# Optimization experiments

Measured on AMD Instinct MI355X. Metric: run time of the kernel, lower is better.

The kernel has to match this reference:

```python
import jax, jax.numpy as jnp
import numpy as np

NUM_FEATURES = 40960
EMB_DIM = 2048


def setup_inputs() -> dict:
    key = jax.random.key(0)
    ks = jax.random.split(key, 8)
    B, L = 4096, 32
    white = jax.random.randint(ks[0], (B, L), 0, NUM_FEATURES, dtype=jnp.int64)
    black = jax.random.randint(ks[1], (B, L), 0, NUM_FEATURES, dtype=jnp.int64)
    stm = jax.random.randint(ks[2], (B,), 0, 2, dtype=jnp.int64)
    emb_table = jax.random.normal(ks[3], (NUM_FEATURES, EMB_DIM), dtype=jnp.float32) * 0.02
    W1 = jax.random.normal(ks[4], (128, 2 * EMB_DIM), dtype=jnp.float32) * 0.02
    b1 = jax.random.normal(ks[5], (128,), dtype=jnp.float32) * 0.02
    W2 = jax.random.normal(ks[6], (1, 128), dtype=jnp.float32) * 0.02
    b2 = jax.random.normal(ks[7], (1,), dtype=jnp.float32) * 0.02
    return {"white": white, "black": black, "stm": stm,
            "emb_table": emb_table, "W1": W1, "b1": b1, "W2": W2, "b2": b2}


def _encode(emb_table, idx):
    # idx: [B, L] padded with 0; embedding gather then mask out padding (index 0)
    emb = emb_table[idx]                         # [B, L, D]
    mask = (idx != 0)[..., None].astype(emb.dtype)
    return (emb * mask).sum(axis=1)              # [B, D]


def reference(white, black, stm, emb_table, W1, b1, W2, b2):
    w = _encode(emb_table, white)                # [B, D]
    b = _encode(emb_table, black)                # [B, D]
    wb = jnp.concatenate([w, b], axis=1)         # [B, 2D]
    bw = jnp.concatenate([b, w], axis=1)
    x = jnp.where((stm == 1)[:, None], wb, bw)
    h = jax.nn.relu(x @ W1.T + b1)               # [B, 128]
    return h @ W2.T + b2                         # [B, 1]
```

## Files before the change

kernel.cpp:

```cpp
#include <hip/hip_runtime.h>
#include <cstddef>

typedef __bf16 bf16x8 __attribute__((ext_vector_type(8)));
typedef float  floatx4 __attribute__((ext_vector_type(4)));

static __device__ __forceinline__ unsigned short f2bf(float f) {
    unsigned int u = __float_as_uint(f);
    u = u + 0x7fff + ((u >> 16) & 1);
    return (unsigned short)(u >> 16);
}
static __device__ __forceinline__ float bflo(unsigned int u) {
    return __uint_as_float(u << 16);
}
static __device__ __forceinline__ float bfhi(unsigned int u) {
    return __uint_as_float(u & 0xffff0000u);
}

__global__ __launch_bounds__(256) void nnue_convw1(
    const float* __restrict__ W1, unsigned short* __restrict__ W1b)
{
    const int i = (blockIdx.x * 256 + threadIdx.x) * 4;
    const float4 v = *reinterpret_cast<const float4*>(W1 + i);
    ushort4 o;
    o.x = f2bf(v.x); o.y = f2bf(v.y); o.z = f2bf(v.z); o.w = f2bf(v.w);
    *reinterpret_cast<ushort4*>(W1b + i) = o;
}

#define LDST 72
__global__ __launch_bounds__(512) void nnue_pgemm(
    const float* __restrict__ emb, const unsigned short* __restrict__ w1b,
    unsigned short* __restrict__ P)
{
    __shared__ unsigned short As[64 * LDST];
    __shared__ unsigned short Bs[256 * LDST];

    const int t    = threadIdx.x;
    const int wid  = t >> 6;
    const int lane = t & 63;
    const int quad = lane >> 4;
    const int l16  = lane & 15;
    const int wm   = wid >> 2;
    const int wn   = wid & 3;
    const int fbase = blockIdx.x * 64;

    floatx4 acc[2][4];
#pragma unroll
    for (int i = 0; i < 2; ++i)
#pragma unroll
        for (int j = 0; j < 4; ++j) acc[i][j] = (floatx4){0.f, 0.f, 0.f, 0.f};

    for (int kc = 0; kc < 2048; kc += 64) {
        __syncthreads();
#pragma unroll
        for (int i = 0; i < 2; ++i) {
            const int c = t + i * 512;
            const int row = c >> 4, cc = c & 15;
            const float4 v = *reinterpret_cast<const float4*>(
                emb + (size_t)(fbase + row) * 2048 + kc + cc * 4);
            ushort4 o;
            o.x = f2bf(v.x); o.y = f2bf(v.y); o.z = f2bf(v.z); o.w = f2bf(v.w);
            *reinterpret_cast<ushort4*>(As + row * LDST + cc * 4) = o;
        }
#pragma unroll
        for (int i = 0; i < 4; ++i) {
            const int c = t + i * 512;
            const int row = c >> 3, cc = c & 7;
            const uint4 v = *reinterpret_cast<const uint4*>(
                w1b + (size_t)(row & 127) * 4096 + (row >> 7) * 2048 + kc + cc * 8);
            *reinterpret_cast<uint4*>(Bs + row * LDST + cc * 8) = v;
        }
        __syncthreads();
#pragma unroll
        for (int kk = 0; kk < 64; kk += 32) {
            const bf16x8 a0 = *reinterpret_cast<const bf16x8*>(
                As + (wm * 32 + l16) * LDST + kk + quad * 8);
            const bf16x8 a1 = *reinterpret_cast<const bf16x8*>(
                As + (wm * 32 + 16 + l16) * LDST + kk + quad * 8);
#pragma unroll
            for (int ni = 0; ni < 4; ++ni) {
                const bf16x8 bb = *reinterpret_cast<const bf16x8*>(
                    Bs + (wn * 64 + ni * 16 + l16) * LDST + kk + quad * 8);
                acc[0][ni] = __builtin_amdgcn_mfma_f32_16x16x32_bf16(a0, bb, acc[0][ni], 0, 0, 0);
                acc[1][ni] = __builtin_amdgcn_mfma_f32_16x16x32_bf16(a1, bb, acc[1][ni], 0, 0, 0);
            }
        }
    }

#pragma unroll
    for (int mi = 0; mi < 2; ++mi) {
#pragma unroll
        for (int ni = 0; ni < 4; ++ni) {
            const int n = wn * 64 + ni * 16 + l16;
#pragma unroll
            for (int r = 0; r < 4; ++r) {
                const int f = fbase + wm * 32 + mi * 16 + quad * 4 + r;
                P[(size_t)f * 256 + n] = f2bf(acc[mi][ni][r]);
            }
        }
    }
}

__global__ __launch_bounds__(256) void nnue_out(
    const int* __restrict__ white, const int* __restrict__ black,
    const int* __restrict__ stm, const unsigned short* __restrict__ P,
    const float* __restrict__ b1, const float* __restrict__ W2,
    const float* __restrict__ b2, float* __restrict__ out)
{
    __shared__ int sW[128], sB[128];
    const int t = threadIdx.x;
    const int bbase = blockIdx.x * 4;
    if (t < 128) sW[t] = white[bbase * 32 + t];
    else         sB[t - 128] = black[bbase * 32 + (t - 128)];
    __syncthreads();

    const int w = t >> 6, lane = t & 63;
    const int b = bbase + w;
    const int offw = (stm[b] != 0) ? 0 : 128;
    const int offb = 128 - offw;
    const int n2 = lane * 2;

    float h0 = 0.f, h1 = 0.f;
#pragma unroll
    for (int i = 0; i < 32; ++i) {
        const int iw = sW[w * 32 + i];
        const unsigned int uw = *reinterpret_cast<const unsigned int*>(
            P + (size_t)iw * 256 + offw + n2);
        const float mw = (iw != 0) ? 1.f : 0.f;
        h0 += bflo(uw) * mw;
        h1 += bfhi(uw) * mw;

        const int ib = sB[w * 32 + i];
        const unsigned int ub = *reinterpret_cast<const unsigned int*>(
            P + (size_t)ib * 256 + offb + n2);
        const float mb = (ib != 0) ? 1.f : 0.f;
        h0 += bflo(ub) * mb;
        h1 += bfhi(ub) * mb;
    }

    h0 += b1[n2];     h1 += b1[n2 + 1];
    h0 = (h0 > 0.f) ? h0 : 0.f;
    h1 = (h1 > 0.f) ? h1 : 0.f;
    float s = h0 * W2[n2] + h1 * W2[n2 + 1];
#pragma unroll
    for (int m = 1; m < 64; m <<= 1) s += __shfl_xor(s, m, 64);
    if (lane == 0) out[b] = s + b2[0];
}

extern "C" void kernel_launch(void* const* d_in, const int* in_sizes, int n_in,
                              void* d_out, int out_size, void* d_ws, size_t ws_size,
                              hipStream_t stream)
{
    const int*   white = (const int*)d_in[0];
    const int*   black = (const int*)d_in[1];
    const int*   stm   = (const int*)d_in[2];
    const float* emb   = (const float*)d_in[3];
    const float* W1    = (const float*)d_in[4];
    const float* b1    = (const float*)d_in[5];
    const float* W2    = (const float*)d_in[6];
    const float* b2    = (const float*)d_in[7];
    float* out = (float*)d_out;

    unsigned short* w1buf = (unsigned short*)d_ws;
    unsigned short* pbuf  = w1buf + (size_t)128 * 4096;

    nnue_convw1<<<512, 256, 0, stream>>>(W1, w1buf);
    nnue_pgemm<<<640, 512, 0, stream>>>(emb, w1buf, pbuf);
    nnue_out<<<1024, 256, 0, stream>>>(white, black, stm, pbuf, b1, W2, b2, out);
}
```

Measured before the change: 525.7 us.

## Retile projection GEMM to 128x128 blocks with direct-to-LDS swizzled W1 loads

```diff
diff --git a/kernel.cpp b/kernel.cpp
--- a/kernel.cpp
+++ b/kernel.cpp
@@ -26,78 +26,91 @@
     *reinterpret_cast<ushort4*>(W1b + i) = o;
 }
 
-#define LDST 72
-__global__ __launch_bounds__(512) void nnue_pgemm(
+#define ALDS 72
+__global__ __launch_bounds__(256) void nnue_pgemm(
     const float* __restrict__ emb, const unsigned short* __restrict__ w1b,
     unsigned short* __restrict__ P)
 {
-    __shared__ unsigned short As[64 * LDST];
-    __shared__ unsigned short Bs[256 * LDST];
+    __shared__ unsigned short As[128 * ALDS];
+    __shared__ unsigned short Bs[128 * 64];
 
     const int t    = threadIdx.x;
     const int wid  = t >> 6;
     const int lane = t & 63;
     const int quad = lane >> 4;
     const int l16  = lane & 15;
-    const int wm   = wid >> 2;
-    const int wn   = wid & 3;
-    const int fbase = blockIdx.x * 64;
+    const int wm   = wid >> 1;
+    const int wn   = wid & 1;
+    const int fbase = (blockIdx.x >> 1) * 128;
+    const int nblk  = blockIdx.x & 1;
 
-    floatx4 acc[2][4];
+    const int bsrc_shorts = (((lane & 7) ^ (lane >> 3)) << 3);
+    const int brow        = lane >> 3;
+
+    floatx4 acc[4][4];
 #pragma unroll
-    for (int i = 0; i < 2; ++i)
+    for (int i = 0; i < 4; ++i)
 #pragma unroll
         for (int j = 0; j < 4; ++j) acc[i][j] = (floatx4){0.f, 0.f, 0.f, 0.f};
 
     for (int kc = 0; kc < 2048; kc += 64) {
         __syncthreads();
 #pragma unroll
-        for (int i = 0; i < 2; ++i) {
-            const int c = t + i * 512;
-            const int row = c >> 4, cc = c & 15;
+        for (int i = 0; i < 4; ++i) {
+            const int c = wid * 4 + i;
+            const int r = c * 8 + brow;
+            const unsigned short* g = w1b + (size_t)r * 4096 + nblk * 2048
+                                    + kc + bsrc_shorts;
+            auto* dst = (__attribute__((address_space(3))) unsigned int*)(Bs + c * 512);
+            __builtin_amdgcn_global_load_lds(
+                (const __attribute__((address_space(1))) unsigned int*)g,
+                dst, 16, 0, 0);
+        }
+#pragma unroll
+        for (int i = 0; i < 8; ++i) {
+            const int cch = t + i * 256;
+            const int row = cch >> 4, cc = cch & 15;
             const float4 v = *reinterpret_cast<const float4*>(
                 emb + (size_t)(fbase + row) * 2048 + kc + cc * 4);
             ushort4 o;
             o.x = f2bf(v.x); o.y = f2bf(v.y); o.z = f2bf(v.z); o.w = f2bf(v.w);
-            *reinterpret_cast<ushort4*>(As + row * LDST + cc * 4) = o;
-        }
-#pragma unroll
-        for (int i = 0; i < 4; ++i) {
-            const int c = t + i * 512;
-            const int row = c >> 3, cc = c & 7;
-            const uint4 v = *reinterpret_cast<const uint4*>(
-                w1b + (size_t)(row & 127) * 4096 + (row >> 7) * 2048 + kc + cc * 8);
-            *reinterpret_cast<uint4*>(Bs + row * LDST + cc * 8) = v;
+            *reinterpret_cast<ushort4*>(As + row * ALDS + cc * 4) = o;
         }
         __syncthreads();
 #pragma unroll
         for (int kk = 0; kk < 64; kk += 32) {
-            const bf16x8 a0 = *reinterpret_cast<const bf16x8*>(
-                As + (wm * 32 + l16) * LDST + kk + quad * 8);
-            const bf16x8 a1 = *reinterpret_cast<const bf16x8*>(
-                As + (wm * 32 + 16 + l16) * LDST + kk + quad * 8);
+            bf16x8 a[4], b[4];
+#pragma unroll
+            for (int mi = 0; mi < 4; ++mi)
+                a[mi] = *reinterpret_cast<const bf16x8*>(
+                    As + (wm * 64 + mi * 16 + l16) * ALDS + kk + quad * 8);
 #pragma unroll
             for (int ni = 0; ni < 4; ++ni) {
-                const bf16x8 bb = *reinterpret_cast<const bf16x8*>(
-                    Bs + (wn * 64 + ni * 16 + l16) * LDST + kk + quad * 8);
-                acc[0][ni] = __builtin_amdgcn_mfma_f32_16x16x32_bf16(a0, bb, acc[0][ni], 0, 0, 0);
-                acc[1][ni] = __builtin_amdgcn_mfma_f32_16x16x32_bf16(a1, bb, acc[1][ni], 0, 0, 0);
+                const int r  = wn * 64 + ni * 16 + l16;
+                const int cb = (kk * 2 + quad * 16) ^ ((r & 7) << 4);
+                b[ni] = *reinterpret_cast<const bf16x8*>(
+                    reinterpret_cast<const char*>(Bs) + r * 128 + cb);
             }
+#pragma unroll
+            for (int mi = 0; mi < 4; ++mi)
+#pragma unroll
+                for (int ni = 0; ni < 4; ++ni)
+                    acc[mi][ni] = __builtin_amdgcn_mfma_f32_16x16x32_bf16(
+                        a[mi], b[ni], acc[mi][ni], 0, 0, 0);
         }
     }
 
 #pragma unroll
-    for (int mi = 0; mi < 2; ++mi) {
+    for (int mi = 0; mi < 4; ++mi)
 #pragma unroll
         for (int ni = 0; ni < 4; ++ni) {
-            const int n = wn * 64 + ni * 16 + l16;
+            const int n = nblk * 128 + wn * 64 + ni * 16 + l16;
 #pragma unroll
             for (int r = 0; r < 4; ++r) {
-                const int f = fbase + wm * 32 + mi * 16 + quad * 4 + r;
+                const int f = fbase + wm * 64 + mi * 16 + quad * 4 + r;
                 P[(size_t)f * 256 + n] = f2bf(acc[mi][ni][r]);
             }
         }
-    }
 }
 
 __global__ __launch_bounds__(256) void nnue_out(
@@ -164,6 +177,6 @@
     unsigned short* pbuf  = w1buf + (size_t)128 * 4096;
 
     nnue_convw1<<<512, 256, 0, stream>>>(W1, w1buf);
-    nnue_pgemm<<<640, 512, 0, stream>>>(emb, w1buf, pbuf);
+    nnue_pgemm<<<640, 256, 0, stream>>>(emb, w1buf, pbuf);
     nnue_out<<<1024, 256, 0, stream>>>(white, black, stm, pbuf, b1, W2, b2, out);
 }
```

New measurement: 524.5 us. About the same (-0.2%).
